# Performance work log

Measured on AMD Instinct MI355X. Metric: run time of the kernel, lower is better.

## Reference

```python
import jax, jax.numpy as jnp
import numpy as np

ROPE_DIMS = 64  # rope_rotary_dims == head_dim, so RoPE covers full head


def fixed_pos_embedding(max_len, rotary_dims):
    inv_freq = 1.0 / (10000 ** (jnp.arange(0, rotary_dims, 2, dtype=jnp.float32) / rotary_dims))
    sinusoid = jnp.einsum('i,j->ij', jnp.arange(max_len, dtype=jnp.float32), inv_freq)
    return jnp.sin(sinusoid), jnp.cos(sinusoid)


def rotate_every_two(x):
    x1 = x[..., ::2]
    x2 = x[..., 1::2]
    return jnp.stack((-x2, x1), axis=-1).reshape(x.shape)


def apply_rotary_pos_emb(x, sin, cos):
    # x: [B, L, H, D]; sin/cos: [L, D//2]
    L = x.shape[1]
    sin = jnp.repeat(sin[:L], 2, axis=-1)[None, :, None, :]  # interleaved repeat == .repeat(2, axis=3)
    cos = jnp.repeat(cos[:L], 2, axis=-1)[None, :, None, :]
    return x * cos + rotate_every_two(x) * sin


def setup_inputs() -> dict:
    key = jax.random.key(0)
    ks = jax.random.split(key, 8)
    B, Lq, Lkv, F, H, D = 2, 2048, 2048, 1024, 16, 64
    s = 0.02
    return {
        'inputs_q': jax.random.normal(ks[0], (B, Lq, F), dtype=jnp.float32),
        'inputs_kv': jax.random.normal(ks[1], (B, Lkv, F), dtype=jnp.float32),
        'mask': jax.random.randint(ks[2], (B, 1, Lq, Lkv), 0, 2) > 0,
        'Wq': jax.random.normal(ks[3], (F, H, D), dtype=jnp.float32) * s,
        'bq': jnp.zeros((H, D), dtype=jnp.float32),
        'Wk': jax.random.normal(ks[4], (F, D), dtype=jnp.float32) * s,
        'bk': jnp.zeros((D,), dtype=jnp.float32),
        'Wv': jax.random.normal(ks[5], (F, D), dtype=jnp.float32) * s,
        'bv': jnp.zeros((D,), dtype=jnp.float32),
        'Wo': jax.random.normal(ks[6], (H, D, F), dtype=jnp.float32) * s,
        'bo': jnp.zeros((F,), dtype=jnp.float32),
    }


def reference(inputs_q, inputs_kv, mask, Wq, bq, Wk, bk, Wv, bv, Wo, bo):
    D = Wq.shape[-1]
    Lq, Lkv = inputs_q.shape[1], inputs_kv.shape[1]
    # QKV projections (multi-query: single shared K/V head)
    q = jnp.einsum('blf,fhd->blhd', inputs_q, Wq) + bq   # [B,Lq,H,D]
    k = jnp.einsum('blf,fd->bld', inputs_kv, Wk) + bk    # [B,Lkv,D]
    v = jnp.einsum('blf,fd->bld', inputs_kv, Wv) + bv    # [B,Lkv,D]
    # RoPE on q and (head-expanded) k
    sin, cos = fixed_pos_embedding(max(Lq, Lkv), ROPE_DIMS)
    q = apply_rotary_pos_emb(q, sin, cos)
    k = apply_rotary_pos_emb(k[:, :, None, :], sin, cos)[:, :, 0, :]
    # multi-query attention
    q = q / jnp.sqrt(jnp.float32(D))
    attn = jnp.einsum('bqhd,bkd->bhqk', q, k)            # [B,H,Lq,Lkv]
    big_neg = jnp.finfo(jnp.float32).min
    attn = jnp.where(mask, attn, big_neg)
    attn = jax.nn.softmax(attn, axis=-1)
    out = jnp.einsum('bhqk,bkd->bqhd', attn, v)          # [B,Lq,H,D]
    # output projection
    return jnp.einsum('bqhd,hdf->bqf', out, Wo) + bo     # [B,Lq,F]
```

## Files before the change

kernel.cpp:

```cpp
#include <hip/hip_runtime.h>

typedef unsigned short u16;
typedef unsigned int u32;
typedef unsigned long long u64;
typedef __bf16 bf16x8 __attribute__((ext_vector_type(8)));
typedef __bf16 bf16x4 __attribute__((ext_vector_type(4)));
typedef u16 u16x8 __attribute__((ext_vector_type(8)));
typedef float f32x4 __attribute__((ext_vector_type(4)));
typedef float f32x16 __attribute__((ext_vector_type(16)));
typedef u32 u32x4 __attribute__((ext_vector_type(4)));

__device__ __forceinline__ u16 f2bf(float f) {
    return __builtin_bit_cast(u16, (__bf16)f);
}

__device__ __forceinline__ void gl_lds16(const void* g, void* l) {
    __builtin_amdgcn_global_load_lds(
        (const __attribute__((address_space(1))) unsigned int*)g,
        (__attribute__((address_space(3))) unsigned int*)l, 16, 0, 0);
}

#define QSCALE 0.18033688011112042f

__global__ void detect_mask(const unsigned char* __restrict__ m, int* __restrict__ flag,
                            float* __restrict__ lut) {
    int t = threadIdx.x;
    lut[t] = (((t >> 2) >> (t & 3)) & 1) ? -16.0f : -100000.0f;
    if (t == 0) {
        int any0 = 0, any1 = 0;
        for (int g = 0; g < 64; ++g) {
            any0 |= (m[4 * g] != 0);
            any1 |= (m[4 * g + 1] != 0);
        }
        *flag = any1 ? 0 : (any0 ? 1 : 2);
    }
}

__global__ void prep(const float4* __restrict__ inq, const float4* __restrict__ inkv,
                     ushort4* __restrict__ oAq, ushort4* __restrict__ oAkv,
                     const float* __restrict__ Wq, const float* __restrict__ Wk,
                     const float* __restrict__ Wv, const float* __restrict__ Wo,
                     u16* __restrict__ Wcat, u16* __restrict__ Wot,
                     const void* __restrict__ mask, const int* __restrict__ flagp,
                     u64* __restrict__ Mb, float2* __restrict__ rtbl) {
    int bid = blockIdx.x;
    const int tid = threadIdx.x;
    if (bid < 8192) {
        int i = bid * 256 + tid;
        const float4* src; ushort4* dst; int j;
        if (i < 1048576) { src = inq;  dst = oAq;  j = i; }
        else             { src = inkv; dst = oAkv; j = i - 1048576; }
        float4 f = src[j];
        ushort4 o;
        o.x = f2bf(f.x); o.y = f2bf(f.y); o.z = f2bf(f.z); o.w = f2bf(f.w);
        dst[j] = o;
        return;
    }
    bid -= 8192;
    if (bid < 2176) {
        const float* src; u16* dst; int C, bx, by;
        if (bid < 1024)      { src = Wq; dst = Wcat;           C = 1024; bx = bid & 31;          by = bid >> 5; }
        else if (bid < 2048) { src = Wo; dst = Wot;            C = 1024; bx = (bid - 1024) & 31; by = (bid - 1024) >> 5; }
        else if (bid < 2112) { src = Wk; dst = Wcat + 1048576; C = 64;   bx = (bid - 2048) & 1;  by = (bid - 2048) >> 1; }
        else                 { src = Wv; dst = Wcat + 1114112; C = 64;   bx = (bid - 2112) & 1;  by = (bid - 2112) >> 1; }
        __shared__ float t[32][33];
        int tx = tid & 31, ty = tid >> 5;
        bx *= 32; by *= 32;
#pragma unroll
        for (int i = 0; i < 4; ++i)
            t[ty + i * 8][tx] = src[(size_t)(by + ty + i * 8) * C + bx + tx];
        __syncthreads();
#pragma unroll
        for (int i = 0; i < 4; ++i)
            dst[(size_t)(bx + ty + i * 8) * 1024 + by + tx] = f2bf(t[tx][ty + i * 8]);
        return;
    }
    bid -= 2176;
    if (bid < 256) {
        int i = bid * 256 + tid;
        int pos = i >> 5, j = i & 31;
        float inv = powf(10000.0f, -(float)(2 * j) * (1.0f / 64.0f));
        float s, c;
        sincosf((float)pos * inv, &s, &c);
        rtbl[i] = make_float2(c, s);
        return;
    }
    bid -= 256;
    {
        int flag = *flagp;
        int lane = tid & 63;
        for (int wid = bid * 4 + (tid >> 6); wid < 131072; wid += 8192) {
            size_t idx = (size_t)wid * 64 + lane;
            bool v;
            if (flag == 0)      v = ((const unsigned char*)mask)[idx] != 0;
            else if (flag == 1) v = ((const int*)mask)[idx] != 0;
            else                v = ((const float*)mask)[idx] != 0.f;
            u64 bm = __ballot(v);
            if (lane == 0) Mb[wid] = bm;
        }
    }
}

template <int MODE>
__launch_bounds__(256)
__global__ void gemm_bt(const u16* __restrict__ A0, const u16* __restrict__ A1,
                        const u16* __restrict__ Bt,
                        const float* __restrict__ b1, const float* __restrict__ b2,
                        const float* __restrict__ b3,
                        const float2* __restrict__ rtbl,
                        u16* __restrict__ oQ, u16* __restrict__ oK, u16* __restrict__ oV,
                        float* __restrict__ oF, int Ntiles) {
    __shared__ __align__(16) u16 lA[2][64 * 64];
    __shared__ __align__(16) u16 lB[2][128 * 64];
    const int tid = threadIdx.x, w = tid >> 6, lane = tid & 63;
    const int tm = blockIdx.x / Ntiles, tn = blockIdx.x % Ntiles;
    const int wm = w >> 1, wn = w & 1;
    const int lq = lane & 15, g = lane >> 4, g4 = g << 2;
    const u32 swz = (lane & 7) << 4;
    const u32 bcolg = (16 * g) ^ swz;
    const u16* A = (MODE == 0 && tn == 8) ? A1 : A0;

    const int rA0 = tid >> 3, ch = tid & 7;
    const u32 offc = ((u32)(ch << 4)) ^ ((u32)((rA0 & 7) << 4));
    const u16* pA0 = A + (size_t)(tm * 64 + rA0) * 1024 + ch * 8;
    const u16* pA1 = pA0 + 32 * 1024;
    const u16* pB0 = Bt + (size_t)(tn * 128 + rA0) * 1024 + ch * 8;
    const u16* pB1 = pB0 + 32 * 1024;
    const u16* pB2 = pB0 + 64 * 1024;
    const u16* pB3 = pB0 + 96 * 1024;
    const u32 offA0 = rA0 * 128 + offc, offA1 = offA0 + 32 * 128;
    const u32 offB0 = offA0, offB1 = offB0 + 32 * 128, offB2 = offB0 + 64 * 128,
              offB3 = offB0 + 96 * 128;

    u16x8 ra0, ra1, rb0, rb1, rb2, rb3;
    f32x4 acc[2][4] = {};

    ra0 = *(const u16x8*)(pA0); ra1 = *(const u16x8*)(pA1);
    rb0 = *(const u16x8*)(pB0); rb1 = *(const u16x8*)(pB1);
    rb2 = *(const u16x8*)(pB2); rb3 = *(const u16x8*)(pB3);
    *(u16x8*)((char*)lA + offA0) = ra0; *(u16x8*)((char*)lA + offA1) = ra1;
    *(u16x8*)((char*)lB + offB0) = rb0; *(u16x8*)((char*)lB + offB1) = rb1;
    *(u16x8*)((char*)lB + offB2) = rb2; *(u16x8*)((char*)lB + offB3) = rb3;
    __syncthreads();

#pragma unroll
    for (int t = 0; t < 16; ++t) {
        if (t < 15) {
            ra0 = *(const u16x8*)(pA0 + (t + 1) * 64); ra1 = *(const u16x8*)(pA1 + (t + 1) * 64);
            rb0 = *(const u16x8*)(pB0 + (t + 1) * 64); rb1 = *(const u16x8*)(pB1 + (t + 1) * 64);
            rb2 = *(const u16x8*)(pB2 + (t + 1) * 64); rb3 = *(const u16x8*)(pB3 + (t + 1) * 64);
        }
        const char* bA = (const char*)lA + (t & 1) * 8192;
        const char* bB = (const char*)lB + (t & 1) * 16384;
#pragma unroll
        for (int kc = 0; kc < 2; ++kc) {
            const u32 col = bcolg ^ (64 * kc);
            bf16x8 af0 = *(const bf16x8*)(bA + (wm * 32 + lq) * 128 + col);
            bf16x8 af1 = *(const bf16x8*)(bA + (wm * 32 + 16 + lq) * 128 + col);
            bf16x8 bg0 = *(const bf16x8*)(bB + (wn * 64 + lq) * 128 + col);
            bf16x8 bg1 = *(const bf16x8*)(bB + (wn * 64 + 16 + lq) * 128 + col);
            bf16x8 bg2 = *(const bf16x8*)(bB + (wn * 64 + 32 + lq) * 128 + col);
            bf16x8 bg3 = *(const bf16x8*)(bB + (wn * 64 + 48 + lq) * 128 + col);
            acc[0][0] = __builtin_amdgcn_mfma_f32_16x16x32_bf16(af0, bg0, acc[0][0], 0, 0, 0);
            acc[0][1] = __builtin_amdgcn_mfma_f32_16x16x32_bf16(af0, bg1, acc[0][1], 0, 0, 0);
            acc[0][2] = __builtin_amdgcn_mfma_f32_16x16x32_bf16(af0, bg2, acc[0][2], 0, 0, 0);
            acc[0][3] = __builtin_amdgcn_mfma_f32_16x16x32_bf16(af0, bg3, acc[0][3], 0, 0, 0);
            acc[1][0] = __builtin_amdgcn_mfma_f32_16x16x32_bf16(af1, bg0, acc[1][0], 0, 0, 0);
            acc[1][1] = __builtin_amdgcn_mfma_f32_16x16x32_bf16(af1, bg1, acc[1][1], 0, 0, 0);
            acc[1][2] = __builtin_amdgcn_mfma_f32_16x16x32_bf16(af1, bg2, acc[1][2], 0, 0, 0);
            acc[1][3] = __builtin_amdgcn_mfma_f32_16x16x32_bf16(af1, bg3, acc[1][3], 0, 0, 0);
        }
        if (t < 15) {
            char* nA = (char*)lA + ((t + 1) & 1) * 8192;
            char* nB = (char*)lB + ((t + 1) & 1) * 16384;
            *(u16x8*)(nA + offA0) = ra0; *(u16x8*)(nA + offA1) = ra1;
            *(u16x8*)(nB + offB0) = rb0; *(u16x8*)(nB + offB1) = rb1;
            *(u16x8*)(nB + offB2) = rb2; *(u16x8*)(nB + offB3) = rb3;
        }
        __syncthreads();
    }

#pragma unroll
    for (int mi = 0; mi < 2; ++mi) {
#pragma unroll
        for (int ni = 0; ni < 4; ++ni) {
#pragma unroll
            for (int r = 0; r < 4; ++r) {
                int grow = tm * 64 + wm * 32 + mi * 16 + g4 + r;
                float v = acc[mi][ni][r];
                if constexpr (MODE == 0) {
                    int pos = grow & 2047;
                    if (tn < 8) {
                        int gcol = tn * 128 + wn * 64 + ni * 16 + lq;
                        v += b1[gcol];
                        float2 cs = rtbl[pos * 32 + ((gcol & 63) >> 1)];
                        float prt = __shfl_xor(v, 1);
                        v = (gcol & 1) ? (v * cs.x + prt * cs.y) : (v * cs.x - prt * cs.y);
                        v *= QSCALE;
                        oQ[(size_t)grow * 1024 + gcol] = f2bf(v);
                    } else {
                        int lc = wn * 64 + ni * 16 + lq;
                        if (lc < 64) {
                            v += b2[lc];
                            float2 cs = rtbl[pos * 32 + (lc >> 1)];
                            float prt = __shfl_xor(v, 1);
                            v = (lc & 1) ? (v * cs.x + prt * cs.y) : (v * cs.x - prt * cs.y);
                            oK[(size_t)grow * 64 + ((((u32)lc >> 2) ^ ((u32)grow & 15)) << 2)
                               + (lc & 3)] = f2bf(v);
                        } else {
                            int d = lc - 64;
                            v += b3[d];
                            int b = grow >> 11, ll = grow & 2047;
                            int cc = ll & 63;
                            oV[((size_t)(b * 64 + d)) * 2048 + (ll & ~63)
                               + ((((u32)cc >> 2) ^ ((u32)d & 15)) << 2) + (cc & 3)] = f2bf(v);
                        }
                    }
                } else {
                    int gcol = tn * 128 + wn * 64 + ni * 16 + lq;
                    oF[(size_t)grow * 1024 + gcol] = v + b1[gcol];
                }
            }
        }
    }
}

#define MFMA32(A, B, C) __builtin_amdgcn_mfma_f32_32x32x16_bf16(A, B, C, 0, 0, 0)

__launch_bounds__(256)
__global__ void flash(const u16* __restrict__ Qb, const u16* __restrict__ Kb,
                      const u16* __restrict__ Vt, const u64* __restrict__ Mb,
                      const f32x4* __restrict__ lut, u16* __restrict__ Ob) {
    __shared__ __align__(16) u16 lK[2][64 * 64];
    __shared__ __align__(16) u16 lV[2][64 * 64];
    const int tid = threadIdx.x, w = tid >> 6, lane = tid & 63;
    const int qt = blockIdx.x & 15, hh = (blockIdx.x >> 4) & 15, b = blockIdx.x >> 8;
    const int qb = qt * 128 + w * 32;
    const int l31 = lane & 31, h = lane >> 5, l15 = lane & 15;

    bf16x8 qf0, qf1, qf2, qf3;
    {
        const u16* qp = Qb + (size_t)(b * 2048 + qb + l31) * 1024 + hh * 64 + h * 8;
        qf0 = *(const bf16x8*)(qp);
        qf1 = *(const bf16x8*)(qp + 16);
        qf2 = *(const bf16x8*)(qp + 32);
        qf3 = *(const bf16x8*)(qp + 48);
    }

    const u64* Mrow = Mb + (size_t)(b * 2048 + qb + l31) * 32;

    u32 dof0 = ((u32)(2 * h) ^ l15) << 3,      dof1 = ((u32)(2 * h + 1) ^ l15) << 3;
    u32 dof2 = ((u32)(4 + 2 * h) ^ l15) << 3,  dof3 = ((u32)(5 + 2 * h) ^ l15) << 3;
    u32 dof4 = ((u32)(8 + 2 * h) ^ l15) << 3,  dof5 = ((u32)(9 + 2 * h) ^ l15) << 3;
    u32 dof6 = ((u32)(12 + 2 * h) ^ l15) << 3, dof7 = ((u32)(13 + 2 * h) ^ l15) << 3;
    const char* kvbase = (const char*)lK + l31 * 128;

    const u16* pK = Kb + (size_t)b * 131072 + tid * 8;
    const u16* pV = Vt + (size_t)(b * 64 + (tid >> 3)) * 2048 + (tid & 7) * 8;
    const u16* pV2 = pV + 32 * 2048;

#define STAGE(BUF)                                                       \
    {                                                                    \
        gl_lds16(pK,        (char*)lK + (BUF) * 8192 + tid * 16);        \
        gl_lds16(pK + 2048, (char*)lK + (BUF) * 8192 + 4096 + tid * 16); \
        gl_lds16(pV,        (char*)lV + (BUF) * 8192 + tid * 16);        \
        gl_lds16(pV2,       (char*)lV + (BUF) * 8192 + 4096 + tid * 16); \
        pK += 4096; pV += 64; pV2 += 64;                                 \
    }

    f32x16 o0 = {}, o1 = {};
    f32x16 cin0, cin1;
    float lsum = 0.f;
    u64 mw;

#define BUILD_CIN(MW)                                                        \
    {                                                                        \
        u64 ms_ = (MW) >> (4 * h);                                           \
        _Pragma("unroll") for (int rg = 0; rg < 4; ++rg) {                   \
            f32x4 e0_ = lut[(u32)((ms_ >> (8 * rg)) & 15)];                  \
            f32x4 e1_ = lut[(u32)((ms_ >> (32 + 8 * rg)) & 15)];             \
            cin0[4 * rg] = e0_[0]; cin0[4 * rg + 1] = e0_[1];                \
            cin0[4 * rg + 2] = e0_[2]; cin0[4 * rg + 3] = e0_[3];            \
            cin1[4 * rg] = e1_[0]; cin1[4 * rg + 1] = e1_[1];                \
            cin1[4 * rg + 2] = e1_[2]; cin1[4 * rg + 3] = e1_[3];            \
        }                                                                    \
    }

#define FRAG(DST, IMM, OFA, OFB)                                             \
    {                                                                        \
        bf16x4 lo_ = *(const bf16x4*)(kvbase + (IMM) + (OFA));               \
        bf16x4 hi_ = *(const bf16x4*)(kvbase + (IMM) + (OFB));               \
        DST = __builtin_shufflevector(lo_, hi_, 0, 1, 2, 3, 4, 5, 6, 7);     \
    }

#define PK2(A, B) ((u32)f2bf(A) | ((u32)f2bf(B) << 16))
#define MKPA(PA, E0, E1, E2, E3, E4, E5, E6, E7)                             \
    {                                                                        \
        u32 x0_ = PK2(E0, E1), x1_ = PK2(E2, E3);                            \
        u32 y0_ = PK2(E4, E5), y1_ = PK2(E6, E7);                            \
        asm("v_permlane32_swap_b32 %0, %1" : "+v"(x0_), "+v"(y0_));          \
        asm("v_permlane32_swap_b32 %0, %1" : "+v"(x1_), "+v"(y1_));          \
        u32x4 t_ = {x0_, x1_, y0_, y1_};                                     \
        PA = __builtin_bit_cast(bf16x8, t_);                                 \
    }

#define CHUNK(BUF, KC)                                                                   \
    {                                                                                    \
        if ((KC) < 31) STAGE((BUF) ^ 1);                                                 \
        f32x16 st0 = cin0, st1 = cin1;                                                   \
        {                                                                                \
            bf16x8 kf;                                                                   \
            FRAG(kf, (BUF) * 8192,        dof0, dof1); st0 = MFMA32(kf, qf0, st0);       \
            FRAG(kf, (BUF) * 8192,        dof2, dof3); st0 = MFMA32(kf, qf1, st0);       \
            FRAG(kf, (BUF) * 8192,        dof4, dof5); st0 = MFMA32(kf, qf2, st0);       \
            FRAG(kf, (BUF) * 8192,        dof6, dof7); st0 = MFMA32(kf, qf3, st0);       \
            FRAG(kf, (BUF) * 8192 + 4096, dof0, dof1); st1 = MFMA32(kf, qf0, st1);       \
            FRAG(kf, (BUF) * 8192 + 4096, dof2, dof3); st1 = MFMA32(kf, qf1, st1);       \
            FRAG(kf, (BUF) * 8192 + 4096, dof4, dof5); st1 = MFMA32(kf, qf2, st1);       \
            FRAG(kf, (BUF) * 8192 + 4096, dof6, dof7); st1 = MFMA32(kf, qf3, st1);       \
        }                                                                                \
        float e0 = exp2f(st0[0]), e1 = exp2f(st0[1]), e2 = exp2f(st0[2]),                \
              e3 = exp2f(st0[3]), e4 = exp2f(st0[4]), e5 = exp2f(st0[5]),                \
              e6 = exp2f(st0[6]), e7 = exp2f(st0[7]), e8 = exp2f(st0[8]),                \
              e9 = exp2f(st0[9]), e10 = exp2f(st0[10]), e11 = exp2f(st0[11]),            \
              e12 = exp2f(st0[12]), e13 = exp2f(st0[13]), e14 = exp2f(st0[14]),          \
              e15 = exp2f(st0[15]);                                                      \
        float f0 = exp2f(st1[0]), f1 = exp2f(st1[1]), f2 = exp2f(st1[2]),                \
              f3 = exp2f(st1[3]), f4 = exp2f(st1[4]), f5 = exp2f(st1[5]),                \
              f6 = exp2f(st1[6]), f7 = exp2f(st1[7]), f8 = exp2f(st1[8]),                \
              f9 = exp2f(st1[9]), f10 = exp2f(st1[10]), f11 = exp2f(st1[11]),            \
              f12 = exp2f(st1[12]), f13 = exp2f(st1[13]), f14 = exp2f(st1[14]),          \
              f15 = exp2f(st1[15]);                                                      \
        lsum += (((e0 + e1) + (e2 + e3)) + ((e4 + e5) + (e6 + e7))) +                    \
                (((e8 + e9) + (e10 + e11)) + ((e12 + e13) + (e14 + e15))) +              \
                (((f0 + f1) + (f2 + f3)) + ((f4 + f5) + (f6 + f7))) +                    \
                (((f8 + f9) + (f10 + f11)) + ((f12 + f13) + (f14 + f15)));               \
        bf16x8 pa0, pa1, pa2, pa3;                                                       \
        MKPA(pa0, e0, e1, e2, e3, e4, e5, e6, e7);                                       \
        MKPA(pa1, e8, e9, e10, e11, e12, e13, e14, e15);                                 \
        MKPA(pa2, f0, f1, f2, f3, f4, f5, f6, f7);                                       \
        MKPA(pa3, f8, f9, f10, f11, f12, f13, f14, f15);                                 \
        BUILD_CIN(mw);                                                                   \
        mw = Mrow[(KC) + 2];                                                             \
        {                                                                                \
            bf16x8 vv;                                                                   \
            FRAG(vv, 16384 + (BUF) * 8192,        dof0, dof1); o0 = MFMA32(pa0, vv, o0); \
            FRAG(vv, 16384 + (BUF) * 8192,        dof2, dof3); o0 = MFMA32(pa1, vv, o0); \
            FRAG(vv, 16384 + (BUF) * 8192,        dof4, dof5); o0 = MFMA32(pa2, vv, o0); \
            FRAG(vv, 16384 + (BUF) * 8192,        dof6, dof7); o0 = MFMA32(pa3, vv, o0); \
            FRAG(vv, 16384 + (BUF) * 8192 + 4096, dof0, dof1); o1 = MFMA32(pa0, vv, o1); \
            FRAG(vv, 16384 + (BUF) * 8192 + 4096, dof2, dof3); o1 = MFMA32(pa1, vv, o1); \
            FRAG(vv, 16384 + (BUF) * 8192 + 4096, dof4, dof5); o1 = MFMA32(pa2, vv, o1); \
            FRAG(vv, 16384 + (BUF) * 8192 + 4096, dof6, dof7); o1 = MFMA32(pa3, vv, o1); \
        }                                                                                \
        __syncthreads();                                                                 \
    }

    STAGE(0);
    mw = Mrow[0];
    BUILD_CIN(mw);
    mw = Mrow[1];
    __syncthreads();

    for (int t2 = 0; t2 < 16; ++t2) {
        CHUNK(0, 2 * t2);
        CHUNK(1, 2 * t2 + 1);
    }
#undef STAGE
#undef CHUNK
#undef BUILD_CIN
#undef FRAG
#undef MKPA
#undef PK2

    lsum += __shfl_xor(lsum, 32);
    float rl = 1.0f / lsum;
    const size_t obase = (size_t)(b * 2048 + qb) * 1024 + hh * 64 + l31;
#pragma unroll
    for (int r = 0; r < 16; ++r) {
        int qloc = (r & 3) + 8 * (r >> 2) + 4 * h;
        float rq = __shfl(rl, qloc);
        Ob[obase + (size_t)qloc * 1024]      = f2bf(o0[r] * rq);
        Ob[obase + (size_t)qloc * 1024 + 32] = f2bf(o1[r] * rq);
    }
}

extern "C" void kernel_launch(void* const* d_in, const int* in_sizes, int n_in,
                              void* d_out, int out_size, void* d_ws, size_t ws_size,
                              hipStream_t stream) {
    (void)in_sizes; (void)n_in; (void)out_size; (void)ws_size;
    const float* inq  = (const float*)d_in[0];
    const float* inkv = (const float*)d_in[1];
    const void*  mask = d_in[2];
    const float* Wq   = (const float*)d_in[3];
    const float* bq   = (const float*)d_in[4];
    const float* Wk   = (const float*)d_in[5];
    const float* bk   = (const float*)d_in[6];
    const float* Wv   = (const float*)d_in[7];
    const float* bv   = (const float*)d_in[8];
    const float* Wo   = (const float*)d_in[9];
    const float* bo   = (const float*)d_in[10];
    float* out = (float*)d_out;

    char* ws = (char*)d_ws;
    int* flag    = (int*)ws;
    f32x4* lut   = (f32x4*)(ws + 256);
    u16* Aq   = (u16*)(ws + 512);
    u16* Akv  = Aq + 4194304;
    u16* Wcat = Akv + 4194304;
    u16* Wot  = Wcat + 1179648;
    u16* Qb   = Wot + 1048576;
    u16* Kbf  = Qb + 4194304;
    u16* Vtb  = Kbf + 266496;
    u16* Ob   = Vtb + 266496;
    u64* Mb   = (u64*)(Ob + 4194304);
    float2* rtbl = (float2*)(Mb + 131080);

    detect_mask<<<1, 64, 0, stream>>>((const unsigned char*)mask, flag, (float*)lut);
    prep<<<12672, 256, 0, stream>>>((const float4*)inq, (const float4*)inkv,
                                    (ushort4*)Aq, (ushort4*)Akv,
                                    Wq, Wk, Wv, Wo, Wcat, Wot,
                                    mask, flag, Mb, rtbl);
    gemm_bt<0><<<576, 256, 0, stream>>>(Aq, Akv, Wcat, bq, bk, bv, rtbl,
                                        Qb, Kbf, Vtb, nullptr, 9);
    flash<<<512, 256, 0, stream>>>(Qb, Kbf, Vtb, Mb, lut, Ob);
    gemm_bt<2><<<512, 256, 0, stream>>>(Ob, nullptr, Wot, bo, nullptr, nullptr, rtbl,
                                        nullptr, nullptr, nullptr, out, 8);
}
```

Before: 153.2 us.

## Split flash attention over KV halves, add combine kernel, use direct-to-LDS loads in GEMM

The attention kernel now splits each query tile's KV range into two halves across separate blocks, doubling the grid. Each block writes unnormalized bf16 partial outputs and row sums, and a new combine kernel sums the halves and normalizes them. The GEMM switches from register-staged global loads to global_load_lds direct-to-LDS loads. Flash also caches the mask LUT in shared memory, builds mask biases inline, adds s_setprio around MFMA blocks and sets launch bounds to 4 waves. The split relies on a fixed-offset softmax with no running max, so summing partials is valid, but bf16 partial outputs add rounding and the combine kernel adds an extra pass over memory.

```diff
diff --git a/kernel.cpp b/kernel.cpp
--- a/kernel.cpp
+++ b/kernel.cpp
@@ -12,6 +12,10 @@
 
 __device__ __forceinline__ u16 f2bf(float f) {
     return __builtin_bit_cast(u16, (__bf16)f);
+}
+__device__ __forceinline__ float bf2f(u16 v) {
+    u32 u = ((u32)v) << 16;
+    return __builtin_bit_cast(float, u);
 }
 
 __device__ __forceinline__ void gl_lds16(const void* g, void* l) {
@@ -120,36 +124,33 @@
     const u32 bcolg = (16 * g) ^ swz;
     const u16* A = (MODE == 0 && tn == 8) ? A1 : A0;
 
-    const int rA0 = tid >> 3, ch = tid & 7;
-    const u32 offc = ((u32)(ch << 4)) ^ ((u32)((rA0 & 7) << 4));
-    const u16* pA0 = A + (size_t)(tm * 64 + rA0) * 1024 + ch * 8;
-    const u16* pA1 = pA0 + 32 * 1024;
-    const u16* pB0 = Bt + (size_t)(tn * 128 + rA0) * 1024 + ch * 8;
-    const u16* pB1 = pB0 + 32 * 1024;
-    const u16* pB2 = pB0 + 64 * 1024;
-    const u16* pB3 = pB0 + 96 * 1024;
-    const u32 offA0 = rA0 * 128 + offc, offA1 = offA0 + 32 * 128;
-    const u32 offB0 = offA0, offB1 = offB0 + 32 * 128, offB2 = offB0 + 64 * 128,
-              offB3 = offB0 + 96 * 128;
-
-    u16x8 ra0, ra1, rb0, rb1, rb2, rb3;
+    const int rs = tid >> 3, ch = tid & 7;
+    const u32 sc = (u32)((ch ^ (rs & 7)) * 8);
+    const u16* gA0 = A + (size_t)(tm * 64 + rs) * 1024 + sc;
+    const u16* gA1 = gA0 + 32 * 1024;
+    const u16* gB0 = Bt + (size_t)(tn * 128 + rs) * 1024 + sc;
+    const u16* gB1 = gB0 + 32 * 1024;
+    const u16* gB2 = gB0 + 64 * 1024;
+    const u16* gB3 = gB0 + 96 * 1024;
+
+#define GSTAGE(BUFI, T)                                                        \
+    {                                                                          \
+        gl_lds16(gA0 + (T) * 64, (char*)lA + (BUFI) * 8192 + tid * 16);        \
+        gl_lds16(gA1 + (T) * 64, (char*)lA + (BUFI) * 8192 + 4096 + tid * 16); \
+        gl_lds16(gB0 + (T) * 64, (char*)lB + (BUFI) * 16384 + tid * 16);       \
+        gl_lds16(gB1 + (T) * 64, (char*)lB + (BUFI) * 16384 + 4096 + tid * 16);\
+        gl_lds16(gB2 + (T) * 64, (char*)lB + (BUFI) * 16384 + 8192 + tid * 16);\
+        gl_lds16(gB3 + (T) * 64, (char*)lB + (BUFI) * 16384 + 12288 + tid * 16);\
+    }
+
     f32x4 acc[2][4] = {};
 
-    ra0 = *(const u16x8*)(pA0); ra1 = *(const u16x8*)(pA1);
-    rb0 = *(const u16x8*)(pB0); rb1 = *(const u16x8*)(pB1);
-    rb2 = *(const u16x8*)(pB2); rb3 = *(const u16x8*)(pB3);
-    *(u16x8*)((char*)lA + offA0) = ra0; *(u16x8*)((char*)lA + offA1) = ra1;
-    *(u16x8*)((char*)lB + offB0) = rb0; *(u16x8*)((char*)lB + offB1) = rb1;
-    *(u16x8*)((char*)lB + offB2) = rb2; *(u16x8*)((char*)lB + offB3) = rb3;
+    GSTAGE(0, 0);
     __syncthreads();
 
 #pragma unroll
     for (int t = 0; t < 16; ++t) {
-        if (t < 15) {
-            ra0 = *(const u16x8*)(pA0 + (t + 1) * 64); ra1 = *(const u16x8*)(pA1 + (t + 1) * 64);
-            rb0 = *(const u16x8*)(pB0 + (t + 1) * 64); rb1 = *(const u16x8*)(pB1 + (t + 1) * 64);
-            rb2 = *(const u16x8*)(pB2 + (t + 1) * 64); rb3 = *(const u16x8*)(pB3 + (t + 1) * 64);
-        }
+        if (t < 15) GSTAGE((t + 1) & 1, t + 1);
         const char* bA = (const char*)lA + (t & 1) * 8192;
         const char* bB = (const char*)lB + (t & 1) * 16384;
 #pragma unroll
@@ -170,15 +171,9 @@
             acc[1][2] = __builtin_amdgcn_mfma_f32_16x16x32_bf16(af1, bg2, acc[1][2], 0, 0, 0);
             acc[1][3] = __builtin_amdgcn_mfma_f32_16x16x32_bf16(af1, bg3, acc[1][3], 0, 0, 0);
         }
-        if (t < 15) {
-            char* nA = (char*)lA + ((t + 1) & 1) * 8192;
-            char* nB = (char*)lB + ((t + 1) & 1) * 16384;
-            *(u16x8*)(nA + offA0) = ra0; *(u16x8*)(nA + offA1) = ra1;
-            *(u16x8*)(nB + offB0) = rb0; *(u16x8*)(nB + offB1) = rb1;
-            *(u16x8*)(nB + offB2) = rb2; *(u16x8*)(nB + offB3) = rb3;
-        }
         __syncthreads();
     }
+#undef GSTAGE
 
 #pragma unroll
     for (int mi = 0; mi < 2; ++mi) {
@@ -227,16 +222,22 @@
 
 #define MFMA32(A, B, C) __builtin_amdgcn_mfma_f32_32x32x16_bf16(A, B, C, 0, 0, 0)
 
-__launch_bounds__(256)
+__launch_bounds__(256, 4)
 __global__ void flash(const u16* __restrict__ Qb, const u16* __restrict__ Kb,
                       const u16* __restrict__ Vt, const u64* __restrict__ Mb,
-                      const f32x4* __restrict__ lut, u16* __restrict__ Ob) {
+                      const f32x4* __restrict__ lut,
+                      u16* __restrict__ oPa, u16* __restrict__ oPb,
+                      float* __restrict__ lsPa, float* __restrict__ lsPb) {
     __shared__ __align__(16) u16 lK[2][64 * 64];
     __shared__ __align__(16) u16 lV[2][64 * 64];
+    __shared__ f32x4 slut[16];
     const int tid = threadIdx.x, w = tid >> 6, lane = tid & 63;
-    const int qt = blockIdx.x & 15, hh = (blockIdx.x >> 4) & 15, b = blockIdx.x >> 8;
+    const int s = blockIdx.x & 1, qt = (blockIdx.x >> 1) & 15;
+    const int hh = (blockIdx.x >> 5) & 15, b = blockIdx.x >> 9;
     const int qb = qt * 128 + w * 32;
     const int l31 = lane & 31, h = lane >> 5, l15 = lane & 15;
+
+    if (tid < 16) slut[tid] = lut[tid];
 
     bf16x8 qf0, qf1, qf2, qf3;
     {
@@ -247,7 +248,7 @@
         qf3 = *(const bf16x8*)(qp + 48);
     }
 
-    const u64* Mrow = Mb + (size_t)(b * 2048 + qb + l31) * 32;
+    const u64* mp = Mb + (size_t)(b * 2048 + qb + l31) * 32 + s * 16;
 
     u32 dof0 = ((u32)(2 * h) ^ l15) << 3,      dof1 = ((u32)(2 * h + 1) ^ l15) << 3;
     u32 dof2 = ((u32)(4 + 2 * h) ^ l15) << 3,  dof3 = ((u32)(5 + 2 * h) ^ l15) << 3;
@@ -255,8 +256,8 @@
     u32 dof6 = ((u32)(12 + 2 * h) ^ l15) << 3, dof7 = ((u32)(13 + 2 * h) ^ l15) << 3;
     const char* kvbase = (const char*)lK + l31 * 128;
 
-    const u16* pK = Kb + (size_t)b * 131072 + tid * 8;
-    const u16* pV = Vt + (size_t)(b * 64 + (tid >> 3)) * 2048 + (tid & 7) * 8;
+    const u16* pK = Kb + (size_t)b * 131072 + (size_t)s * 65536 + tid * 8;
+    const u16* pV = Vt + (size_t)(b * 64 + (tid >> 3)) * 2048 + s * 1024 + (tid & 7) * 8;
     const u16* pV2 = pV + 32 * 2048;
 
 #define STAGE(BUF)                                                       \
@@ -269,22 +270,8 @@
     }
 
     f32x16 o0 = {}, o1 = {};
-    f32x16 cin0, cin1;
     float lsum = 0.f;
-    u64 mw;
-
-#define BUILD_CIN(MW)                                                        \
-    {                                                                        \
-        u64 ms_ = (MW) >> (4 * h);                                           \
-        _Pragma("unroll") for (int rg = 0; rg < 4; ++rg) {                   \
-            f32x4 e0_ = lut[(u32)((ms_ >> (8 * rg)) & 15)];                  \
-            f32x4 e1_ = lut[(u32)((ms_ >> (32 + 8 * rg)) & 15)];             \
-            cin0[4 * rg] = e0_[0]; cin0[4 * rg + 1] = e0_[1];                \
-            cin0[4 * rg + 2] = e0_[2]; cin0[4 * rg + 3] = e0_[3];            \
-            cin1[4 * rg] = e1_[0]; cin1[4 * rg + 1] = e1_[1];                \
-            cin1[4 * rg + 2] = e1_[2]; cin1[4 * rg + 3] = e1_[3];            \
-        }                                                                    \
-    }
+    u64 mwc;
 
 #define FRAG(DST, IMM, OFA, OFB)                                             \
     {                                                                        \
@@ -304,10 +291,31 @@
         PA = __builtin_bit_cast(bf16x8, t_);                                 \
     }
 
-#define CHUNK(BUF, KC)                                                                   \
+#define CHUNK(BUF, KCL, LAST)                                                            \
     {                                                                                    \
-        if ((KC) < 31) STAGE((BUF) ^ 1);                                                 \
-        f32x16 st0 = cin0, st1 = cin1;                                                   \
+        if (!(LAST)) STAGE((BUF) ^ 1);                                                   \
+        u64 ms_ = mwc >> (4 * h);                                                        \
+        mwc = mp[(KCL) + 1];                                                             \
+        f32x16 st0, st1;                                                                 \
+        {                                                                                \
+            f32x4 e0_ = slut[(u32)(ms_) & 15];                                           \
+            f32x4 e1_ = slut[(u32)(ms_ >> 8) & 15];                                      \
+            f32x4 e2_ = slut[(u32)(ms_ >> 16) & 15];                                     \
+            f32x4 e3_ = slut[(u32)(ms_ >> 24) & 15];                                     \
+            f32x4 g0_ = slut[(u32)(ms_ >> 32) & 15];                                     \
+            f32x4 g1_ = slut[(u32)(ms_ >> 40) & 15];                                     \
+            f32x4 g2_ = slut[(u32)(ms_ >> 48) & 15];                                     \
+            f32x4 g3_ = slut[(u32)(ms_ >> 56) & 15];                                     \
+            st0[0] = e0_[0]; st0[1] = e0_[1]; st0[2] = e0_[2]; st0[3] = e0_[3];          \
+            st0[4] = e1_[0]; st0[5] = e1_[1]; st0[6] = e1_[2]; st0[7] = e1_[3];          \
+            st0[8] = e2_[0]; st0[9] = e2_[1]; st0[10] = e2_[2]; st0[11] = e2_[3];        \
+            st0[12] = e3_[0]; st0[13] = e3_[1]; st0[14] = e3_[2]; st0[15] = e3_[3];      \
+            st1[0] = g0_[0]; st1[1] = g0_[1]; st1[2] = g0_[2]; st1[3] = g0_[3];          \
+            st1[4] = g1_[0]; st1[5] = g1_[1]; st1[6] = g1_[2]; st1[7] = g1_[3];          \
+            st1[8] = g2_[0]; st1[9] = g2_[1]; st1[10] = g2_[2]; st1[11] = g2_[3];        \
+            st1[12] = g3_[0]; st1[13] = g3_[1]; st1[14] = g3_[2]; st1[15] = g3_[3];      \
+        }                                                                                \
+        __builtin_amdgcn_s_setprio(1);                                                   \
         {                                                                                \
             bf16x8 kf;                                                                   \
             FRAG(kf, (BUF) * 8192,        dof0, dof1); st0 = MFMA32(kf, qf0, st0);       \
@@ -319,6 +327,7 @@
             FRAG(kf, (BUF) * 8192 + 4096, dof4, dof5); st1 = MFMA32(kf, qf2, st1);       \
             FRAG(kf, (BUF) * 8192 + 4096, dof6, dof7); st1 = MFMA32(kf, qf3, st1);       \
         }                                                                                \
+        __builtin_amdgcn_s_setprio(0);                                                   \
         float e0 = exp2f(st0[0]), e1 = exp2f(st0[1]), e2 = exp2f(st0[2]),                \
               e3 = exp2f(st0[3]), e4 = exp2f(st0[4]), e5 = exp2f(st0[5]),                \
               e6 = exp2f(st0[6]), e7 = exp2f(st0[7]), e8 = exp2f(st0[8]),                \
@@ -340,8 +349,7 @@
         MKPA(pa1, e8, e9, e10, e11, e12, e13, e14, e15);                                 \
         MKPA(pa2, f0, f1, f2, f3, f4, f5, f6, f7);                                       \
         MKPA(pa3, f8, f9, f10, f11, f12, f13, f14, f15);                                 \
-        BUILD_CIN(mw);                                                                   \
-        mw = Mrow[(KC) + 2];                                                             \
+        __builtin_amdgcn_s_setprio(1);                                                   \
         {                                                                                \
             bf16x8 vv;                                                                   \
             FRAG(vv, 16384 + (BUF) * 8192,        dof0, dof1); o0 = MFMA32(pa0, vv, o0); \
@@ -353,36 +361,55 @@
             FRAG(vv, 16384 + (BUF) * 8192 + 4096, dof4, dof5); o1 = MFMA32(pa2, vv, o1); \
             FRAG(vv, 16384 + (BUF) * 8192 + 4096, dof6, dof7); o1 = MFMA32(pa3, vv, o1); \
         }                                                                                \
+        __builtin_amdgcn_s_setprio(0);                                                   \
         __syncthreads();                                                                 \
     }
 
     STAGE(0);
-    mw = Mrow[0];
-    BUILD_CIN(mw);
-    mw = Mrow[1];
+    mwc = mp[0];
     __syncthreads();
 
-    for (int t2 = 0; t2 < 16; ++t2) {
-        CHUNK(0, 2 * t2);
-        CHUNK(1, 2 * t2 + 1);
+    for (int t2 = 0; t2 < 8; ++t2) {
+        CHUNK(0, 2 * t2, false);
+        CHUNK(1, 2 * t2 + 1, t2 == 7);
     }
 #undef STAGE
 #undef CHUNK
-#undef BUILD_CIN
 #undef FRAG
 #undef MKPA
 #undef PK2
 
     lsum += __shfl_xor(lsum, 32);
-    float rl = 1.0f / lsum;
-    const size_t obase = (size_t)(b * 2048 + qb) * 1024 + hh * 64 + l31;
+    u16* op = (s ? oPb : oPa) + (size_t)(b * 2048 + qb) * 1024 + hh * 64 + l31;
+    if (h == 0) {
+        float* lp = (s ? lsPb : lsPa);
+        lp[(b * 16 + hh) * 2048 + qb + l31] = lsum;
+    }
 #pragma unroll
     for (int r = 0; r < 16; ++r) {
         int qloc = (r & 3) + 8 * (r >> 2) + 4 * h;
-        float rq = __shfl(rl, qloc);
-        Ob[obase + (size_t)qloc * 1024]      = f2bf(o0[r] * rq);
-        Ob[obase + (size_t)qloc * 1024 + 32] = f2bf(o1[r] * rq);
-    }
+        op[(size_t)qloc * 1024]      = f2bf(o0[r]);
+        op[(size_t)qloc * 1024 + 32] = f2bf(o1[r]);
+    }
+}
+
+__global__ void combine(const ushort4* __restrict__ pa, const ushort4* __restrict__ pb,
+                        const float* __restrict__ la, const float* __restrict__ lb,
+                        ushort4* __restrict__ Ob) {
+    int i = blockIdx.x * 256 + threadIdx.x;
+    int row = i >> 8;
+    int col = (i & 255) * 4;
+    int hh = col >> 6;
+    int b = row >> 11, q = row & 2047;
+    ushort4 x = pa[i], y = pb[i];
+    int li = (b * 16 + hh) * 2048 + q;
+    float rl = 1.0f / (la[li] + lb[li]);
+    ushort4 o;
+    o.x = f2bf((bf2f(x.x) + bf2f(y.x)) * rl);
+    o.y = f2bf((bf2f(x.y) + bf2f(y.y)) * rl);
+    o.z = f2bf((bf2f(x.z) + bf2f(y.z)) * rl);
+    o.w = f2bf((bf2f(x.w) + bf2f(y.w)) * rl);
+    Ob[i] = o;
 }
 
 extern "C" void kernel_launch(void* const* d_in, const int* in_sizes, int n_in,
@@ -416,6 +443,11 @@
     u64* Mb   = (u64*)(Ob + 4194304);
     float2* rtbl = (float2*)(Mb + 131080);
 
+    u16* oPa = Aq;
+    u16* oPb = Akv;
+    float* lsPa = (float*)Wcat;
+    float* lsPb = lsPa + 65536;
+
     detect_mask<<<1, 64, 0, stream>>>((const unsigned char*)mask, flag, (float*)lut);
     prep<<<12672, 256, 0, stream>>>((const float4*)inq, (const float4*)inkv,
                                     (ushort4*)Aq, (ushort4*)Akv,
@@ -423,7 +455,9 @@
                                     mask, flag, Mb, rtbl);
     gemm_bt<0><<<576, 256, 0, stream>>>(Aq, Akv, Wcat, bq, bk, bv, rtbl,
                                         Qb, Kbf, Vtb, nullptr, 9);
-    flash<<<512, 256, 0, stream>>>(Qb, Kbf, Vtb, Mb, lut, Ob);
+    flash<<<1024, 256, 0, stream>>>(Qb, Kbf, Vtb, Mb, lut, oPa, oPb, lsPa, lsPb);
+    combine<<<4096, 256, 0, stream>>>((const ushort4*)oPa, (const ushort4*)oPb,
+                                      lsPa, lsPb, (ushort4*)Ob);
     gemm_bt<2><<<512, 256, 0, stream>>>(Ob, nullptr, Wot, bo, nullptr, nullptr, rtbl,
                                         nullptr, nullptr, nullptr, out, 8);
 }
```

Result: slower. 193.8 us (+26.5%).
